# Performance work log

Measured on AMD Instinct MI355X. Metric: run time of the kernel, lower is better.

Reference implementation:

```python
import jax, jax.numpy as jnp
import numpy as np

DIM = 512
HID = 4 * DIM
E = 8
B, T = 2, 2048


def setup_inputs() -> dict:
    key = jax.random.key(0)
    ks = jax.random.split(key, 8)
    s = 0.02
    x = jax.random.normal(ks[0], (B, T, DIM), dtype=jnp.float32)
    route = jax.random.randint(ks[1], (B * T,), 0, E, dtype=jnp.int32)
    # stacked per-expert params; Linear y = x @ W + b with W in [in, out] layout
    w_in = jax.random.normal(ks[2], (E, DIM, HID), dtype=jnp.float32) * s
    b_in = jnp.zeros((E, HID), dtype=jnp.float32)
    w_gate = jax.random.normal(ks[3], (E, DIM, HID), dtype=jnp.float32) * s
    b_gate = jnp.zeros((E, HID), dtype=jnp.float32)
    w_out = jax.random.normal(ks[4], (E, HID, DIM), dtype=jnp.float32) * s
    b_out = jnp.zeros((E, DIM), dtype=jnp.float32)
    return {"x": x, "route": route, "w_in": w_in, "b_in": b_in,
            "w_gate": w_gate, "b_gate": b_gate, "w_out": w_out, "b_out": b_out}


def reference(x, route, w_in, b_in, w_gate, b_gate, w_out, b_out):
    Bb, Tt, C = x.shape
    xf = x.reshape(-1, C)  # [N, C]
    out = jnp.zeros_like(xf)
    n_experts = w_in.shape[0]
    # loop over the small fixed expert set; each expert is a SwiGLU FFN,
    # output scattered back by masking (same math as output[idx] += expert(x[idx]))
    for e in range(n_experts):
        mask = (route == e).astype(xf.dtype)[:, None]  # [N, 1]
        h = jax.nn.silu(xf @ w_gate[e] + b_gate[e]) * (xf @ w_in[e] + b_in[e])  # [N, 4C]
        out = out + mask * (h @ w_out[e] + b_out[e])
    return out.reshape(Bb, Tt, C)
```

## Files before the change

### kernel.cpp

```cpp
#include <hip/hip_runtime.h>

#define DIM 512
#define HID 2048
#define NEXP 8

typedef __attribute__((ext_vector_type(8))) short v8s;
typedef __attribute__((ext_vector_type(4))) float v4f;

__device__ __forceinline__ unsigned short f2bf(float f) {
  union { __bf16 b; unsigned short u; } c;
  c.b = (__bf16)f;
  return c.u;
}

__device__ __forceinline__ void gload16(const void* g, void* l) {
  __builtin_amdgcn_global_load_lds(
      (const __attribute__((address_space(1))) unsigned int*)g,
      (__attribute__((address_space(3))) unsigned int*)l, 16, 0, 0);
}

__global__ void route_prep(const int* __restrict__ route, int* __restrict__ meta, int ntok) {
  __shared__ int c[NEXP];
  int t = threadIdx.x;
  if (t < NEXP) c[t] = 0;
  __syncthreads();
  for (int n = t; n < ntok; n += blockDim.x) atomicAdd(&c[route[n]], 1);
  __syncthreads();
  if (t == 0) {
    int acc = 0, pacc = 0;
    for (int e = 0; e < NEXP; ++e) {
      meta[e] = c[e];
      meta[NEXP + e] = acc;
      meta[2 * NEXP + e] = acc;
      meta[3 * NEXP + e] = pacc;
      acc += c[e];
      pacc += ((c[e] + 127) >> 7) << 7;
    }
  }
}

__global__ void fill_perm(const int* __restrict__ route, int* __restrict__ meta,
                          int* __restrict__ perm, int ntok) {
  int n = blockIdx.x * blockDim.x + threadIdx.x;
  if (n < ntok) {
    int p = atomicAdd(&meta[2 * NEXP + route[n]], 1);
    perm[p] = n;
  }
}


__global__ __launch_bounds__(256) void wgi_conv(
    const float* __restrict__ wg, const float* __restrict__ wi,
    unsigned short* __restrict__ wgp, unsigned short* __restrict__ wip)
{
  const int s = blockIdx.x;
  const int j = blockIdx.y;
  const int e = blockIdx.z >> 1;
  const int which = blockIdx.z & 1;
  const float* src = (which ? wi : wg) + (size_t)e * DIM * HID;
  unsigned short* dst = (which ? wip : wgp) + (((size_t)e * 16 + j) * 8 + s) * 8192;
  const int t = threadIdx.x;
  #pragma unroll
  for (int i = 0; i < 4; ++i) {
    const int c = t + 256 * i;
    const int kq = c >> 7, n = c & 127;
    const float* srow = src + (size_t)(s * 64 + kq * 8) * HID + j * 128 + n;
    v8s r;
    #pragma unroll
    for (int q = 0; q < 8; ++q) r[q] = (short)f2bf(srow[(size_t)q * HID]);
    *(v8s*)(dst + (size_t)c * 8) = r;
  }
}

__global__ __launch_bounds__(256) void wo_conv(
    const float* __restrict__ wo, unsigned short* __restrict__ wop)
{
  const int s = blockIdx.x;
  const int j = blockIdx.y;
  const int e = blockIdx.z;
  const float* src = wo + (size_t)e * HID * DIM;
  unsigned short* dst = wop + (((size_t)e * 8 + j) * 32 + s) * 4096;
  const int t = threadIdx.x;
  #pragma unroll
  for (int i = 0; i < 2; ++i) {
    const int c = t + 256 * i;
    const int kq = c >> 6, n = c & 63;
    const float* srow = src + (size_t)(s * 64 + kq * 8) * DIM + j * 64 + n;
    v8s r;
    #pragma unroll
    for (int q = 0; q < 8; ++q) r[q] = (short)f2bf(srow[(size_t)q * DIM]);
    *(v8s*)(dst + (size_t)c * 8) = r;
  }
}

__global__ __launch_bounds__(256) void x_conv(
    const float* __restrict__ x, const int* __restrict__ meta,
    const int* __restrict__ perm, unsigned short* __restrict__ xp)
{
  const int bid = blockIdx.x;
  const int e = bid & 7;
  const int mt = bid >> 3;
  const int cnt = meta[e];
  if (mt * 64 >= cnt) return;
  const int off  = meta[NEXP + e];
  const int poff = meta[3 * NEXP + e];
  const int t = threadIdx.x;
  const int r = t & 63, q = t >> 6;
  int arow = mt * 64 + r; if (arow >= cnt) arow = cnt - 1;
  const float* src = x + (size_t)perm[off + arow] * DIM + q * 128;
  unsigned short* dst = xp + (size_t)((poff + mt * 64) >> 6) * 32768;
  #pragma unroll
  for (int j = 0; j < 16; ++j) {
    float4 f0 = ((const float4*)src)[2 * j];
    float4 f1 = ((const float4*)src)[2 * j + 1];
    v8s v;
    v[0] = (short)f2bf(f0.x); v[1] = (short)f2bf(f0.y);
    v[2] = (short)f2bf(f0.z); v[3] = (short)f2bf(f0.w);
    v[4] = (short)f2bf(f1.x); v[5] = (short)f2bf(f1.y);
    v[6] = (short)f2bf(f1.z); v[7] = (short)f2bf(f1.w);
    *(v8s*)(dst + (size_t)((q * 16 + j) * 64 + r) * 8) = v;
  }
}

__global__ __launch_bounds__(256, 4) void gemm1(
    const unsigned short* __restrict__ xp,
    const unsigned short* __restrict__ wgp, const float* __restrict__ bg_,
    const unsigned short* __restrict__ wip, const float* __restrict__ bi_,
    const int* __restrict__ meta,
    unsigned short* __restrict__ hbuf)
{
  const int bid = blockIdx.x;
  const int e = bid & 7;
  const int r_ = bid >> 3;
  const int j = r_ & 15;
  const int mt = r_ >> 4;
  const int cnt = meta[e];
  const int m0 = mt * 64;
  if (m0 >= cnt) return;
  const int poff = meta[3 * NEXP + e];
  const int n0 = j * 128;

  __shared__ __align__(16) unsigned char lds[40960];

  const int t = threadIdx.x;
  const int l = t & 63, w = t >> 6;
  const int wm = w >> 1, wn = w & 1;
  const int fr = l & 15, fg = l >> 4;

  const unsigned short* pa = xp + (size_t)((poff + m0) >> 6) * 32768;
  const unsigned short* pg = wgp + ((size_t)e * 16 + j) * 65536;
  const unsigned short* pi = wip + ((size_t)e * 16 + j) * 65536;

  v4f accG[2][4], accI[2][4];
  #pragma unroll
  for (int i = 0; i < 2; ++i)
    #pragma unroll
    for (int q = 0; q < 4; ++q) {
      accG[i][q] = (v4f){0.f, 0.f, 0.f, 0.f};
      accI[i][q] = (v4f){0.f, 0.f, 0.f, 0.f};
    }

  auto stage = [&](int s, int b) {
    unsigned char* base = lds + b * 20480;
    gload16(pa + (size_t)s * 2048 + t * 8,        base + w * 1024);
    gload16(pg + (size_t)s * 4096 + t * 8,        base + 4096 + w * 1024);
    gload16(pg + (size_t)s * 4096 + 2048 + t * 8, base + 8192 + w * 1024);
    gload16(pi + (size_t)s * 4096 + t * 8,        base + 12288 + w * 1024);
    gload16(pi + (size_t)s * 4096 + 2048 + t * 8, base + 16384 + w * 1024);
  };

  stage(0, 0);
  __syncthreads();

  int cur = 0;
  for (int s = 0; s < 16; ++s) {
    if (s < 15) stage(s + 1, cur ^ 1);
    unsigned char* base = lds + cur * 20480;
    v8s af[2], gf[4], inf[4];
    #pragma unroll
    for (int mf = 0; mf < 2; ++mf)
      af[mf] = *(const v8s*)(base + ((fg * 64) + wm * 32 + mf * 16 + fr) * 16);
    #pragma unroll
    for (int nf = 0; nf < 4; ++nf) {
      gf[nf]  = *(const v8s*)(base + 4096  + ((fg * 128) + wn * 64 + nf * 16 + fr) * 16);
      inf[nf] = *(const v8s*)(base + 12288 + ((fg * 128) + wn * 64 + nf * 16 + fr) * 16);
    }
    #pragma unroll
    for (int mf = 0; mf < 2; ++mf)
      #pragma unroll
      for (int nf = 0; nf < 4; ++nf) {
        accG[mf][nf] = __builtin_amdgcn_mfma_f32_16x16x32_bf16(af[mf], gf[nf],  accG[mf][nf], 0, 0, 0);
        accI[mf][nf] = __builtin_amdgcn_mfma_f32_16x16x32_bf16(af[mf], inf[nf], accI[mf][nf], 0, 0, 0);
      }
    __syncthreads();
    cur ^= 1;
  }

  const size_t tbase = (size_t)((poff + m0) >> 6) * 131072;
  #pragma unroll
  for (int nf = 0; nf < 4; ++nf) {
    const int c = n0 + wn * 64 + nf * 16 + fr;
    const float bg = bg_[(size_t)e * HID + c];
    const float bi = bi_[(size_t)e * HID + c];
    #pragma unroll
    for (int mf = 0; mf < 2; ++mf)
      #pragma unroll
      for (int jj = 0; jj < 4; ++jj) {
        const int r = wm * 32 + mf * 16 + fg * 4 + jj;
        if (m0 + r < cnt) {
          const float g = accG[mf][nf][jj] + bg;
          const float v = accI[mf][nf][jj] + bi;
          const float hval = g / (1.f + __expf(-g)) * v;
          hbuf[tbase + (size_t)((c >> 3) * 64 + r) * 8 + (c & 7)] = f2bf(hval);
        }
      }
  }
}

__global__ __launch_bounds__(512, 4) void gemm2(
    const unsigned short* __restrict__ hbuf,
    const unsigned short* __restrict__ wop, const float* __restrict__ bo_,
    const int* __restrict__ meta, const int* __restrict__ perm,
    float* __restrict__ out)
{
  const int bid = blockIdx.x;
  const int e = bid & 7;
  const int r_ = bid >> 3;
  const int jn = r_ & 7;
  const int mt = r_ >> 3;
  const int cnt = meta[e];
  const int m0 = mt * 64;
  if (m0 >= cnt) return;
  const int off  = meta[NEXP + e];
  const int poff = meta[3 * NEXP + e];
  const int n0 = jn * 64;

  __shared__ __align__(16) unsigned char lds[32768];

  const int t = threadIdx.x;
  const int l = t & 63, w = t >> 6;
  const int wm = w >> 2, wn = w & 3;
  const int fr = l & 15, fg = l >> 4;

  const unsigned short* pa = hbuf + (size_t)((poff + m0) >> 6) * 131072;
  const unsigned short* pb = wop + ((size_t)e * 8 + jn) * 131072;

  v4f acc[2];
  acc[0] = (v4f){0.f, 0.f, 0.f, 0.f};
  acc[1] = (v4f){0.f, 0.f, 0.f, 0.f};

  auto stage = [&](int s, int b) {
    unsigned char* base = lds + b * 16384;
    gload16(pa + (size_t)s * 4096 + t * 8, base + w * 1024);
    gload16(pb + (size_t)s * 4096 + t * 8, base + 8192 + w * 1024);
  };

  stage(0, 0);
  __syncthreads();

  int cur = 0;
  for (int s = 0; s < 32; ++s) {
    if (s < 31) stage(s + 1, cur ^ 1);
    unsigned char* base = lds + cur * 16384;
    v8s af[2][2], bf2[2];
    #pragma unroll
    for (int kk = 0; kk < 2; ++kk) {
      #pragma unroll
      for (int mf = 0; mf < 2; ++mf)
        af[kk][mf] = *(const v8s*)(base + ((kk * 4 + fg) * 64 + wm * 32 + mf * 16 + fr) * 16);
      bf2[kk] = *(const v8s*)(base + 8192 + ((kk * 4 + fg) * 64 + wn * 16 + fr) * 16);
    }
    #pragma unroll
    for (int kk = 0; kk < 2; ++kk)
      #pragma unroll
      for (int mf = 0; mf < 2; ++mf)
        acc[mf] = __builtin_amdgcn_mfma_f32_16x16x32_bf16(af[kk][mf], bf2[kk], acc[mf], 0, 0, 0);
    __syncthreads();
    cur ^= 1;
  }

  const int c = n0 + wn * 16 + fr;
  const float bo = bo_[(size_t)e * DIM + c];
  #pragma unroll
  for (int mf = 0; mf < 2; ++mf)
    #pragma unroll
    for (int jj = 0; jj < 4; ++jj) {
      const int r = wm * 32 + mf * 16 + fg * 4 + jj;
      if (m0 + r < cnt)
        out[(size_t)perm[off + m0 + r] * DIM + c] = acc[mf][jj] + bo;
    }
}

extern "C" void kernel_launch(void* const* d_in, const int* in_sizes, int n_in,
                              void* d_out, int out_size, void* d_ws, size_t ws_size,
                              hipStream_t stream) {
  const float* x      = (const float*)d_in[0];
  const int*   route  = (const int*)d_in[1];
  const float* w_in   = (const float*)d_in[2];
  const float* b_in   = (const float*)d_in[3];
  const float* w_gate = (const float*)d_in[4];
  const float* b_gate = (const float*)d_in[5];
  const float* w_out  = (const float*)d_in[6];
  const float* b_out  = (const float*)d_in[7];
  float* out = (float*)d_out;

  const int ntok = in_sizes[1];

  int* meta = (int*)d_ws;
  int* perm = (int*)((char*)d_ws + 128);

  const size_t WGP_OFF = 32768;
  const size_t WMAT_BYTES = (size_t)NEXP * DIM * HID * 2;

  unsigned short* wgp  = (unsigned short*)((char*)d_ws + WGP_OFF);
  unsigned short* wip  = (unsigned short*)((char*)d_ws + WGP_OFF + WMAT_BYTES);
  unsigned short* wop  = (unsigned short*)((char*)d_ws + WGP_OFF + 2 * WMAT_BYTES);
  unsigned short* xp   = wop;
  unsigned short* hbuf = (unsigned short*)((char*)d_ws + WGP_OFF + 3 * WMAT_BYTES);

  const int MT64 = (ntok + 63) / 64;

  route_prep<<<1, 256, 0, stream>>>(route, meta, ntok);
  fill_perm<<<(ntok + 255) / 256, 256, 0, stream>>>(route, meta, perm, ntok);
  x_conv<<<NEXP * MT64, 256, 0, stream>>>(x, meta, perm, xp);
  wgi_conv<<<dim3(8, 16, 16), 256, 0, stream>>>(w_gate, w_in, wgp, wip);
  gemm1<<<NEXP * 16 * MT64, 256, 0, stream>>>(
      xp, wgp, b_gate, wip, b_in, meta, hbuf);
  wo_conv<<<dim3(32, 8, 8), 256, 0, stream>>>(w_out, wop);
  gemm2<<<NEXP * 8 * MT64, 512, 0, stream>>>(
      hbuf, wop, b_out, meta, perm, out);
}
```

Measured before the change: 112.9 us.

## Fuse gate/in weight conversion into persistent LDS-resident gemm1 and enlarge gemm2 tiles

```diff
diff --git a/kernel.cpp b/kernel.cpp
--- a/kernel.cpp
+++ b/kernel.cpp
@@ -45,51 +45,6 @@
   if (n < ntok) {
     int p = atomicAdd(&meta[2 * NEXP + route[n]], 1);
     perm[p] = n;
-  }
-}
-
-
-__global__ __launch_bounds__(256) void wgi_conv(
-    const float* __restrict__ wg, const float* __restrict__ wi,
-    unsigned short* __restrict__ wgp, unsigned short* __restrict__ wip)
-{
-  const int s = blockIdx.x;
-  const int j = blockIdx.y;
-  const int e = blockIdx.z >> 1;
-  const int which = blockIdx.z & 1;
-  const float* src = (which ? wi : wg) + (size_t)e * DIM * HID;
-  unsigned short* dst = (which ? wip : wgp) + (((size_t)e * 16 + j) * 8 + s) * 8192;
-  const int t = threadIdx.x;
-  #pragma unroll
-  for (int i = 0; i < 4; ++i) {
-    const int c = t + 256 * i;
-    const int kq = c >> 7, n = c & 127;
-    const float* srow = src + (size_t)(s * 64 + kq * 8) * HID + j * 128 + n;
-    v8s r;
-    #pragma unroll
-    for (int q = 0; q < 8; ++q) r[q] = (short)f2bf(srow[(size_t)q * HID]);
-    *(v8s*)(dst + (size_t)c * 8) = r;
-  }
-}
-
-__global__ __launch_bounds__(256) void wo_conv(
-    const float* __restrict__ wo, unsigned short* __restrict__ wop)
-{
-  const int s = blockIdx.x;
-  const int j = blockIdx.y;
-  const int e = blockIdx.z;
-  const float* src = wo + (size_t)e * HID * DIM;
-  unsigned short* dst = wop + (((size_t)e * 8 + j) * 32 + s) * 4096;
-  const int t = threadIdx.x;
-  #pragma unroll
-  for (int i = 0; i < 2; ++i) {
-    const int c = t + 256 * i;
-    const int kq = c >> 6, n = c & 63;
-    const float* srow = src + (size_t)(s * 64 + kq * 8) * DIM + j * 64 + n;
-    v8s r;
-    #pragma unroll
-    for (int q = 0; q < 8; ++q) r[q] = (short)f2bf(srow[(size_t)q * DIM]);
-    *(v8s*)(dst + (size_t)c * 8) = r;
   }
 }
 
@@ -122,102 +77,141 @@
   }
 }
 
-__global__ __launch_bounds__(256, 4) void gemm1(
+__global__ __launch_bounds__(256) void wo_conv(
+    const float* __restrict__ wo, unsigned short* __restrict__ wop)
+{
+  const int s = blockIdx.x;
+  const int j = blockIdx.y;
+  const int e = blockIdx.z;
+  const float* src = wo + (size_t)e * HID * DIM;
+  unsigned short* dst = wop + (((size_t)e * 8 + j) * 32 + s) * 4096;
+  const int t = threadIdx.x;
+  #pragma unroll
+  for (int i = 0; i < 2; ++i) {
+    const int c = t + 256 * i;
+    const int kq = c >> 6, n = c & 63;
+    const float* srow = src + (size_t)(s * 64 + kq * 8) * DIM + j * 64 + n;
+    v8s r;
+    #pragma unroll
+    for (int q = 0; q < 8; ++q) r[q] = (short)f2bf(srow[(size_t)q * DIM]);
+    *(v8s*)(dst + (size_t)c * 8) = r;
+  }
+}
+
+__global__ __launch_bounds__(256, 1) void gemm1f(
     const unsigned short* __restrict__ xp,
-    const unsigned short* __restrict__ wgp, const float* __restrict__ bg_,
-    const unsigned short* __restrict__ wip, const float* __restrict__ bi_,
+    const float* __restrict__ wg_, const float* __restrict__ bg_,
+    const float* __restrict__ wi_, const float* __restrict__ bi_,
     const int* __restrict__ meta,
     unsigned short* __restrict__ hbuf)
 {
   const int bid = blockIdx.x;
   const int e = bid & 7;
-  const int r_ = bid >> 3;
-  const int j = r_ & 15;
-  const int mt = r_ >> 4;
+  const int j = bid >> 3;
+  const int n0 = j * 64;
   const int cnt = meta[e];
-  const int m0 = mt * 64;
-  if (m0 >= cnt) return;
   const int poff = meta[3 * NEXP + e];
-  const int n0 = j * 128;
-
-  __shared__ __align__(16) unsigned char lds[40960];
+
+  __shared__ __align__(16) unsigned char lds[163840];
 
   const int t = threadIdx.x;
   const int l = t & 63, w = t >> 6;
-  const int wm = w >> 1, wn = w & 1;
   const int fr = l & 15, fg = l >> 4;
 
-  const unsigned short* pa = xp + (size_t)((poff + m0) >> 6) * 32768;
-  const unsigned short* pg = wgp + ((size_t)e * 16 + j) * 65536;
-  const unsigned short* pi = wip + ((size_t)e * 16 + j) * 65536;
-
-  v4f accG[2][4], accI[2][4];
-  #pragma unroll
-  for (int i = 0; i < 2; ++i)
-    #pragma unroll
-    for (int q = 0; q < 4; ++q) {
-      accG[i][q] = (v4f){0.f, 0.f, 0.f, 0.f};
-      accI[i][q] = (v4f){0.f, 0.f, 0.f, 0.f};
-    }
-
-  auto stage = [&](int s, int b) {
-    unsigned char* base = lds + b * 20480;
-    gload16(pa + (size_t)s * 2048 + t * 8,        base + w * 1024);
-    gload16(pg + (size_t)s * 4096 + t * 8,        base + 4096 + w * 1024);
-    gload16(pg + (size_t)s * 4096 + 2048 + t * 8, base + 8192 + w * 1024);
-    gload16(pi + (size_t)s * 4096 + t * 8,        base + 12288 + w * 1024);
-    gload16(pi + (size_t)s * 4096 + 2048 + t * 8, base + 16384 + w * 1024);
-  };
-
-  stage(0, 0);
+  {
+    const float* wg = wg_ + (size_t)e * DIM * HID + n0 + l;
+    const float* wi = wi_ + (size_t)e * DIM * HID + n0 + l;
+    #pragma unroll 4
+    for (int it = 0; it < 16; ++it) {
+      const int kq = w + 4 * it;
+      const float* s0 = wg + (size_t)(kq * 8) * HID;
+      const float* s1 = wi + (size_t)(kq * 8) * HID;
+      v8s r0, r1;
+      #pragma unroll
+      for (int q = 0; q < 8; ++q) {
+        r0[q] = (short)f2bf(s0[(size_t)q * HID]);
+        r1[q] = (short)f2bf(s1[(size_t)q * HID]);
+      }
+      *(v8s*)(lds + (kq * 64 + l) * 16) = r0;
+      *(v8s*)(lds + 65536 + (kq * 64 + l) * 16) = r1;
+    }
+  }
   __syncthreads();
 
-  int cur = 0;
-  for (int s = 0; s < 16; ++s) {
-    if (s < 15) stage(s + 1, cur ^ 1);
-    unsigned char* base = lds + cur * 20480;
-    v8s af[2], gf[4], inf[4];
-    #pragma unroll
-    for (int mf = 0; mf < 2; ++mf)
-      af[mf] = *(const v8s*)(base + ((fg * 64) + wm * 32 + mf * 16 + fr) * 16);
+  unsigned char* xlds = lds + 131072;
+  const int tile0 = poff >> 6;
+  const int nmt = (cnt + 255) >> 8;
+
+  for (int mt = 0; mt < nmt; ++mt) {
+    const int m0 = mt * 256;
+    const size_t xbase = (size_t)(tile0 + (m0 >> 6)) * 32768;
+
+    auto stage_x = [&](int s, int b) {
+      #pragma unroll
+      for (int i = 0; i < 4; ++i)
+        gload16(xp + xbase + (size_t)w * 32768 + ((s * 4 + i) * 64 + l) * 8,
+                xlds + b * 16384 + (w * 64 + 256 * i) * 16);
+    };
+
+    stage_x(0, 0);
+    __syncthreads();
+
+    v4f aG[4][4], aI[4][4];
+    #pragma unroll
+    for (int i = 0; i < 4; ++i)
+      #pragma unroll
+      for (int q = 0; q < 4; ++q) {
+        aG[i][q] = (v4f){0.f, 0.f, 0.f, 0.f};
+        aI[i][q] = (v4f){0.f, 0.f, 0.f, 0.f};
+      }
+
+    int cur = 0;
+    for (int s = 0; s < 16; ++s) {
+      if (s < 15) stage_x(s + 1, cur ^ 1);
+      const unsigned char* xb = xlds + cur * 16384;
+      v8s af[4], gf[4], inf[4];
+      #pragma unroll
+      for (int mf = 0; mf < 4; ++mf)
+        af[mf] = *(const v8s*)(xb + (fg * 256 + w * 64 + mf * 16 + fr) * 16);
+      #pragma unroll
+      for (int nf = 0; nf < 4; ++nf) {
+        gf[nf]  = *(const v8s*)(lds + ((s * 4 + fg) * 64 + nf * 16 + fr) * 16);
+        inf[nf] = *(const v8s*)(lds + 65536 + ((s * 4 + fg) * 64 + nf * 16 + fr) * 16);
+      }
+      #pragma unroll
+      for (int mf = 0; mf < 4; ++mf)
+        #pragma unroll
+        for (int nf = 0; nf < 4; ++nf) {
+          aG[mf][nf] = __builtin_amdgcn_mfma_f32_16x16x32_bf16(af[mf], gf[nf],  aG[mf][nf], 0, 0, 0);
+          aI[mf][nf] = __builtin_amdgcn_mfma_f32_16x16x32_bf16(af[mf], inf[nf], aI[mf][nf], 0, 0, 0);
+        }
+      __syncthreads();
+      cur ^= 1;
+    }
+
     #pragma unroll
     for (int nf = 0; nf < 4; ++nf) {
-      gf[nf]  = *(const v8s*)(base + 4096  + ((fg * 128) + wn * 64 + nf * 16 + fr) * 16);
-      inf[nf] = *(const v8s*)(base + 12288 + ((fg * 128) + wn * 64 + nf * 16 + fr) * 16);
-    }
-    #pragma unroll
-    for (int mf = 0; mf < 2; ++mf)
-      #pragma unroll
-      for (int nf = 0; nf < 4; ++nf) {
-        accG[mf][nf] = __builtin_amdgcn_mfma_f32_16x16x32_bf16(af[mf], gf[nf],  accG[mf][nf], 0, 0, 0);
-        accI[mf][nf] = __builtin_amdgcn_mfma_f32_16x16x32_bf16(af[mf], inf[nf], accI[mf][nf], 0, 0, 0);
-      }
-    __syncthreads();
-    cur ^= 1;
-  }
-
-  const size_t tbase = (size_t)((poff + m0) >> 6) * 131072;
-  #pragma unroll
-  for (int nf = 0; nf < 4; ++nf) {
-    const int c = n0 + wn * 64 + nf * 16 + fr;
-    const float bg = bg_[(size_t)e * HID + c];
-    const float bi = bi_[(size_t)e * HID + c];
-    #pragma unroll
-    for (int mf = 0; mf < 2; ++mf)
-      #pragma unroll
-      for (int jj = 0; jj < 4; ++jj) {
-        const int r = wm * 32 + mf * 16 + fg * 4 + jj;
-        if (m0 + r < cnt) {
-          const float g = accG[mf][nf][jj] + bg;
-          const float v = accI[mf][nf][jj] + bi;
-          const float hval = g / (1.f + __expf(-g)) * v;
-          hbuf[tbase + (size_t)((c >> 3) * 64 + r) * 8 + (c & 7)] = f2bf(hval);
+      const int c = n0 + nf * 16 + fr;
+      const float bg = bg_[(size_t)e * HID + c];
+      const float bi = bi_[(size_t)e * HID + c];
+      #pragma unroll
+      for (int mf = 0; mf < 4; ++mf)
+        #pragma unroll
+        for (int jj = 0; jj < 4; ++jj) {
+          const int r = w * 64 + mf * 16 + fg * 4 + jj;
+          if (m0 + r < cnt) {
+            const float g = aG[mf][nf][jj] + bg;
+            const float v = aI[mf][nf][jj] + bi;
+            const float hval = g / (1.f + __expf(-g)) * v;
+            const int grow = poff + m0 + r;
+            hbuf[(size_t)(grow >> 6) * 131072 + ((c >> 3) * 64 + (grow & 63)) * 8 + (c & 7)] = f2bf(hval);
+          }
         }
-      }
-  }
-}
-
-__global__ __launch_bounds__(512, 4) void gemm2(
+    }
+  }
+}
+
+__global__ __launch_bounds__(256, 3) void gemm2n(
     const unsigned short* __restrict__ hbuf,
     const unsigned short* __restrict__ wop, const float* __restrict__ bo_,
     const int* __restrict__ meta, const int* __restrict__ perm,
@@ -229,30 +223,40 @@
   const int jn = r_ & 7;
   const int mt = r_ >> 3;
   const int cnt = meta[e];
-  const int m0 = mt * 64;
+  const int m0 = mt * 128;
   if (m0 >= cnt) return;
-  const int off  = meta[NEXP + e];
-  const int poff = meta[3 * NEXP + e];
+  const int off = meta[NEXP + e], poff = meta[3 * NEXP + e];
   const int n0 = jn * 64;
 
-  __shared__ __align__(16) unsigned char lds[32768];
+  __shared__ __align__(16) unsigned char lds[49152];
 
   const int t = threadIdx.x;
   const int l = t & 63, w = t >> 6;
-  const int wm = w >> 2, wn = w & 3;
+  const int wm = w >> 1, wn = w & 1;
   const int fr = l & 15, fg = l >> 4;
 
-  const unsigned short* pa = hbuf + (size_t)((poff + m0) >> 6) * 131072;
+  const size_t abase = (size_t)((poff + m0) >> 6) * 131072;
   const unsigned short* pb = wop + ((size_t)e * 8 + jn) * 131072;
 
-  v4f acc[2];
-  acc[0] = (v4f){0.f, 0.f, 0.f, 0.f};
-  acc[1] = (v4f){0.f, 0.f, 0.f, 0.f};
+  v4f acc[4][2];
+  #pragma unroll
+  for (int i = 0; i < 4; ++i) {
+    acc[i][0] = (v4f){0.f, 0.f, 0.f, 0.f};
+    acc[i][1] = (v4f){0.f, 0.f, 0.f, 0.f};
+  }
 
   auto stage = [&](int s, int b) {
-    unsigned char* base = lds + b * 16384;
-    gload16(pa + (size_t)s * 4096 + t * 8, base + w * 1024);
-    gload16(pb + (size_t)s * 4096 + t * 8, base + 8192 + w * 1024);
+    unsigned char* base = lds + b * 24576;
+    #pragma unroll
+    for (int i = 0; i < 4; ++i) {
+      const int kq = (4 * i + w) >> 1;
+      gload16(hbuf + abase + (size_t)(w & 1) * 131072 + ((s * 8 + kq) * 64 + l) * 8,
+              base + (w * 64 + 256 * i) * 16);
+    }
+    #pragma unroll
+    for (int i = 0; i < 2; ++i)
+      gload16(pb + (size_t)s * 4096 + (t + 256 * i) * 8,
+              base + 16384 + (w * 64 + 256 * i) * 16);
   };
 
   stage(0, 0);
@@ -261,34 +265,41 @@
   int cur = 0;
   for (int s = 0; s < 32; ++s) {
     if (s < 31) stage(s + 1, cur ^ 1);
-    unsigned char* base = lds + cur * 16384;
-    v8s af[2][2], bf2[2];
+    unsigned char* base = lds + cur * 24576;
+    v8s af[2][4], bf[2][2];
     #pragma unroll
     for (int kk = 0; kk < 2; ++kk) {
       #pragma unroll
-      for (int mf = 0; mf < 2; ++mf)
-        af[kk][mf] = *(const v8s*)(base + ((kk * 4 + fg) * 64 + wm * 32 + mf * 16 + fr) * 16);
-      bf2[kk] = *(const v8s*)(base + 8192 + ((kk * 4 + fg) * 64 + wn * 16 + fr) * 16);
+      for (int mf = 0; mf < 4; ++mf)
+        af[kk][mf] = *(const v8s*)(base + ((kk * 4 + fg) * 128 + wm * 64 + mf * 16 + fr) * 16);
+      #pragma unroll
+      for (int nf = 0; nf < 2; ++nf)
+        bf[kk][nf] = *(const v8s*)(base + 16384 + ((kk * 4 + fg) * 64 + wn * 32 + nf * 16 + fr) * 16);
     }
     #pragma unroll
     for (int kk = 0; kk < 2; ++kk)
       #pragma unroll
-      for (int mf = 0; mf < 2; ++mf)
-        acc[mf] = __builtin_amdgcn_mfma_f32_16x16x32_bf16(af[kk][mf], bf2[kk], acc[mf], 0, 0, 0);
+      for (int mf = 0; mf < 4; ++mf)
+        #pragma unroll
+        for (int nf = 0; nf < 2; ++nf)
+          acc[mf][nf] = __builtin_amdgcn_mfma_f32_16x16x32_bf16(af[kk][mf], bf[kk][nf], acc[mf][nf], 0, 0, 0);
     __syncthreads();
     cur ^= 1;
   }
 
-  const int c = n0 + wn * 16 + fr;
-  const float bo = bo_[(size_t)e * DIM + c];
   #pragma unroll
-  for (int mf = 0; mf < 2; ++mf)
-    #pragma unroll
-    for (int jj = 0; jj < 4; ++jj) {
-      const int r = wm * 32 + mf * 16 + fg * 4 + jj;
-      if (m0 + r < cnt)
-        out[(size_t)perm[off + m0 + r] * DIM + c] = acc[mf][jj] + bo;
-    }
+  for (int nf = 0; nf < 2; ++nf) {
+    const int c = n0 + wn * 32 + nf * 16 + fr;
+    const float bo = bo_[(size_t)e * DIM + c];
+    #pragma unroll
+    for (int mf = 0; mf < 4; ++mf)
+      #pragma unroll
+      for (int jj = 0; jj < 4; ++jj) {
+        const int r = wm * 64 + mf * 16 + fg * 4 + jj;
+        if (m0 + r < cnt)
+          out[(size_t)perm[off + m0 + r] * DIM + c] = acc[mf][nf][jj] + bo;
+      }
+  }
 }
 
 extern "C" void kernel_launch(void* const* d_in, const int* in_sizes, int n_in,
@@ -309,24 +320,19 @@
   int* meta = (int*)d_ws;
   int* perm = (int*)((char*)d_ws + 128);
 
-  const size_t WGP_OFF = 32768;
-  const size_t WMAT_BYTES = (size_t)NEXP * DIM * HID * 2;
-
-  unsigned short* wgp  = (unsigned short*)((char*)d_ws + WGP_OFF);
-  unsigned short* wip  = (unsigned short*)((char*)d_ws + WGP_OFF + WMAT_BYTES);
-  unsigned short* wop  = (unsigned short*)((char*)d_ws + WGP_OFF + 2 * WMAT_BYTES);
-  unsigned short* xp   = wop;
-  unsigned short* hbuf = (unsigned short*)((char*)d_ws + WGP_OFF + 3 * WMAT_BYTES);
-
-  const int MT64 = (ntok + 63) / 64;
+  unsigned short* xp   = (unsigned short*)((char*)d_ws + 65536);
+  unsigned short* wop  = (unsigned short*)((char*)d_ws + 65536 + 5242880);
+  unsigned short* hbuf = (unsigned short*)((char*)d_ws + 65536 + 5242880 + 33554432);
+
+  const int MT64  = (ntok + 63) / 64;
+  const int MT128 = (ntok + 127) / 128;
 
   route_prep<<<1, 256, 0, stream>>>(route, meta, ntok);
   fill_perm<<<(ntok + 255) / 256, 256, 0, stream>>>(route, meta, perm, ntok);
   x_conv<<<NEXP * MT64, 256, 0, stream>>>(x, meta, perm, xp);
-  wgi_conv<<<dim3(8, 16, 16), 256, 0, stream>>>(w_gate, w_in, wgp, wip);
-  gemm1<<<NEXP * 16 * MT64, 256, 0, stream>>>(
-      xp, wgp, b_gate, wip, b_in, meta, hbuf);
+  gemm1f<<<NEXP * 32, 256, 0, stream>>>(
+      xp, w_gate, b_gate, w_in, b_in, meta, hbuf);
   wo_conv<<<dim3(32, 8, 8), 256, 0, stream>>>(w_out, wop);
-  gemm2<<<NEXP * 8 * MT64, 512, 0, stream>>>(
+  gemm2n<<<NEXP * 8 * MT128, 256, 0, stream>>>(
       hbuf, wop, b_out, meta, perm, out);
 }
```

New measurement: 124.9 us. 10.6% more time.

## Fuse fp32-to-bf16 weight conversion into the expert GEMM load stages

Applied to the files above, without the earlier changes.

```diff
diff --git a/kernel.cpp b/kernel.cpp
--- a/kernel.cpp
+++ b/kernel.cpp
@@ -45,51 +45,6 @@
   if (n < ntok) {
     int p = atomicAdd(&meta[2 * NEXP + route[n]], 1);
     perm[p] = n;
-  }
-}
-
-
-__global__ __launch_bounds__(256) void wgi_conv(
-    const float* __restrict__ wg, const float* __restrict__ wi,
-    unsigned short* __restrict__ wgp, unsigned short* __restrict__ wip)
-{
-  const int s = blockIdx.x;
-  const int j = blockIdx.y;
-  const int e = blockIdx.z >> 1;
-  const int which = blockIdx.z & 1;
-  const float* src = (which ? wi : wg) + (size_t)e * DIM * HID;
-  unsigned short* dst = (which ? wip : wgp) + (((size_t)e * 16 + j) * 8 + s) * 8192;
-  const int t = threadIdx.x;
-  #pragma unroll
-  for (int i = 0; i < 4; ++i) {
-    const int c = t + 256 * i;
-    const int kq = c >> 7, n = c & 127;
-    const float* srow = src + (size_t)(s * 64 + kq * 8) * HID + j * 128 + n;
-    v8s r;
-    #pragma unroll
-    for (int q = 0; q < 8; ++q) r[q] = (short)f2bf(srow[(size_t)q * HID]);
-    *(v8s*)(dst + (size_t)c * 8) = r;
-  }
-}
-
-__global__ __launch_bounds__(256) void wo_conv(
-    const float* __restrict__ wo, unsigned short* __restrict__ wop)
-{
-  const int s = blockIdx.x;
-  const int j = blockIdx.y;
-  const int e = blockIdx.z;
-  const float* src = wo + (size_t)e * HID * DIM;
-  unsigned short* dst = wop + (((size_t)e * 8 + j) * 32 + s) * 4096;
-  const int t = threadIdx.x;
-  #pragma unroll
-  for (int i = 0; i < 2; ++i) {
-    const int c = t + 256 * i;
-    const int kq = c >> 6, n = c & 63;
-    const float* srow = src + (size_t)(s * 64 + kq * 8) * DIM + j * 64 + n;
-    v8s r;
-    #pragma unroll
-    for (int q = 0; q < 8; ++q) r[q] = (short)f2bf(srow[(size_t)q * DIM]);
-    *(v8s*)(dst + (size_t)c * 8) = r;
   }
 }
 
@@ -122,10 +77,10 @@
   }
 }
 
-__global__ __launch_bounds__(256, 4) void gemm1(
+__global__ __launch_bounds__(256, 3) void gemm1r(
     const unsigned short* __restrict__ xp,
-    const unsigned short* __restrict__ wgp, const float* __restrict__ bg_,
-    const unsigned short* __restrict__ wip, const float* __restrict__ bi_,
+    const float* __restrict__ wg_, const float* __restrict__ bg_,
+    const float* __restrict__ wi_, const float* __restrict__ bi_,
     const int* __restrict__ meta,
     unsigned short* __restrict__ hbuf)
 {
@@ -148,55 +103,82 @@
   const int fr = l & 15, fg = l >> 4;
 
   const unsigned short* pa = xp + (size_t)((poff + m0) >> 6) * 32768;
-  const unsigned short* pg = wgp + ((size_t)e * 16 + j) * 65536;
-  const unsigned short* pi = wip + ((size_t)e * 16 + j) * 65536;
-
-  v4f accG[2][4], accI[2][4];
+  const float* wg = wg_ + (size_t)e * DIM * HID + n0;
+  const float* wi = wi_ + (size_t)e * DIM * HID + n0;
+
+  const int s_kq = t >> 7;
+  const int s_n  = t & 127;
+
+  v4f aG[2][4], aI[2][4];
   #pragma unroll
   for (int i = 0; i < 2; ++i)
     #pragma unroll
     for (int q = 0; q < 4; ++q) {
-      accG[i][q] = (v4f){0.f, 0.f, 0.f, 0.f};
-      accI[i][q] = (v4f){0.f, 0.f, 0.f, 0.f};
-    }
-
-  auto stage = [&](int s, int b) {
+      aG[i][q] = (v4f){0.f, 0.f, 0.f, 0.f};
+      aI[i][q] = (v4f){0.f, 0.f, 0.f, 0.f};
+    }
+
+  float stG0[8], stG1[8], stI0[8], stI1[8];
+
+  auto wload = [&](int s) {
+    const size_t b0 = (size_t)(s * 32 + s_kq * 8) * HID + s_n;
+    const size_t b1 = (size_t)(s * 32 + (s_kq + 2) * 8) * HID + s_n;
+    #pragma unroll
+    for (int q = 0; q < 8; ++q) {
+      stG0[q] = wg[b0 + (size_t)q * HID];
+      stG1[q] = wg[b1 + (size_t)q * HID];
+      stI0[q] = wi[b0 + (size_t)q * HID];
+      stI1[q] = wi[b1 + (size_t)q * HID];
+    }
+  };
+  auto wstore = [&](int b) {
     unsigned char* base = lds + b * 20480;
-    gload16(pa + (size_t)s * 2048 + t * 8,        base + w * 1024);
-    gload16(pg + (size_t)s * 4096 + t * 8,        base + 4096 + w * 1024);
-    gload16(pg + (size_t)s * 4096 + 2048 + t * 8, base + 8192 + w * 1024);
-    gload16(pi + (size_t)s * 4096 + t * 8,        base + 12288 + w * 1024);
-    gload16(pi + (size_t)s * 4096 + 2048 + t * 8, base + 16384 + w * 1024);
-  };
-
-  stage(0, 0);
+    v8s g0, g1, i0, i1;
+    #pragma unroll
+    for (int q = 0; q < 8; ++q) {
+      g0[q] = (short)f2bf(stG0[q]); g1[q] = (short)f2bf(stG1[q]);
+      i0[q] = (short)f2bf(stI0[q]); i1[q] = (short)f2bf(stI1[q]);
+    }
+    *(v8s*)(base + 4096  + (s_kq * 128 + s_n) * 16)       = g0;
+    *(v8s*)(base + 4096  + ((s_kq + 2) * 128 + s_n) * 16) = g1;
+    *(v8s*)(base + 12288 + (s_kq * 128 + s_n) * 16)       = i0;
+    *(v8s*)(base + 12288 + ((s_kq + 2) * 128 + s_n) * 16) = i1;
+  };
+  auto aload = [&](int s, int b) {
+    gload16(pa + ((size_t)(s * 4 + w) * 64 + l) * 8, lds + b * 20480 + t * 16);
+  };
+
+  wload(0);
+  aload(0, 0);
+  wstore(0);
   __syncthreads();
 
   int cur = 0;
   for (int s = 0; s < 16; ++s) {
-    if (s < 15) stage(s + 1, cur ^ 1);
-    unsigned char* base = lds + cur * 20480;
+    if (s < 15) { wload(s + 1); aload(s + 1, cur ^ 1); }
+    const unsigned char* base = lds + cur * 20480;
     v8s af[2], gf[4], inf[4];
     #pragma unroll
     for (int mf = 0; mf < 2; ++mf)
-      af[mf] = *(const v8s*)(base + ((fg * 64) + wm * 32 + mf * 16 + fr) * 16);
+      af[mf] = *(const v8s*)(base + (fg * 64 + wm * 32 + mf * 16 + fr) * 16);
     #pragma unroll
     for (int nf = 0; nf < 4; ++nf) {
-      gf[nf]  = *(const v8s*)(base + 4096  + ((fg * 128) + wn * 64 + nf * 16 + fr) * 16);
-      inf[nf] = *(const v8s*)(base + 12288 + ((fg * 128) + wn * 64 + nf * 16 + fr) * 16);
+      gf[nf]  = *(const v8s*)(base + 4096  + (fg * 128 + wn * 64 + nf * 16 + fr) * 16);
+      inf[nf] = *(const v8s*)(base + 12288 + (fg * 128 + wn * 64 + nf * 16 + fr) * 16);
     }
     #pragma unroll
     for (int mf = 0; mf < 2; ++mf)
       #pragma unroll
       for (int nf = 0; nf < 4; ++nf) {
-        accG[mf][nf] = __builtin_amdgcn_mfma_f32_16x16x32_bf16(af[mf], gf[nf],  accG[mf][nf], 0, 0, 0);
-        accI[mf][nf] = __builtin_amdgcn_mfma_f32_16x16x32_bf16(af[mf], inf[nf], accI[mf][nf], 0, 0, 0);
+        aG[mf][nf] = __builtin_amdgcn_mfma_f32_16x16x32_bf16(af[mf], gf[nf],  aG[mf][nf], 0, 0, 0);
+        aI[mf][nf] = __builtin_amdgcn_mfma_f32_16x16x32_bf16(af[mf], inf[nf], aI[mf][nf], 0, 0, 0);
       }
+    if (s < 15) wstore(cur ^ 1);
     __syncthreads();
     cur ^= 1;
   }
 
-  const size_t tbase = (size_t)((poff + m0) >> 6) * 131072;
+  const size_t tb = (size_t)((poff + m0) >> 6) * 131072;
   #pragma unroll
   for (int nf = 0; nf < 4; ++nf) {
     const int c = n0 + wn * 64 + nf * 16 + fr;
@@ -207,74 +189,89 @@
       #pragma unroll
       for (int jj = 0; jj < 4; ++jj) {
         const int r = wm * 32 + mf * 16 + fg * 4 + jj;
-        if (m0 + r < cnt) {
-          const float g = accG[mf][nf][jj] + bg;
-          const float v = accI[mf][nf][jj] + bi;
-          const float hval = g / (1.f + __expf(-g)) * v;
-          hbuf[tbase + (size_t)((c >> 3) * 64 + r) * 8 + (c & 7)] = f2bf(hval);
-        }
+        const float g = aG[mf][nf][jj] + bg;
+        const float v = aI[mf][nf][jj] + bi;
+        const float hval = g / (1.f + __expf(-g)) * v;
+        hbuf[tb + (size_t)((c >> 3) * 64 + r) * 8 + (c & 7)] = f2bf(hval);
       }
   }
 }
 
-__global__ __launch_bounds__(512, 4) void gemm2(
+__global__ __launch_bounds__(256, 4) void gemm2r(
     const unsigned short* __restrict__ hbuf,
-    const unsigned short* __restrict__ wop, const float* __restrict__ bo_,
+    const float* __restrict__ wo_, const float* __restrict__ bo_,
     const int* __restrict__ meta, const int* __restrict__ perm,
     float* __restrict__ out)
 {
   const int bid = blockIdx.x;
   const int e = bid & 7;
   const int r_ = bid >> 3;
-  const int jn = r_ & 7;
-  const int mt = r_ >> 3;
+  const int jn = r_ & 15;
+  const int mt = r_ >> 4;
   const int cnt = meta[e];
   const int m0 = mt * 64;
   if (m0 >= cnt) return;
-  const int off  = meta[NEXP + e];
-  const int poff = meta[3 * NEXP + e];
-  const int n0 = jn * 64;
-
-  __shared__ __align__(16) unsigned char lds[32768];
+  const int off = meta[NEXP + e], poff = meta[3 * NEXP + e];
+  const int n0 = jn * 32;
+
+  __shared__ __align__(16) unsigned char lds[24576];
 
   const int t = threadIdx.x;
   const int l = t & 63, w = t >> 6;
-  const int wm = w >> 2, wn = w & 3;
+  const int wm = w >> 1, wn = w & 1;
   const int fr = l & 15, fg = l >> 4;
 
   const unsigned short* pa = hbuf + (size_t)((poff + m0) >> 6) * 131072;
-  const unsigned short* pb = wop + ((size_t)e * 8 + jn) * 131072;
+  const float* wo = wo_ + (size_t)e * HID * DIM + n0;
+
+  const int b_kq = t >> 5, b_n = t & 31;
 
   v4f acc[2];
   acc[0] = (v4f){0.f, 0.f, 0.f, 0.f};
   acc[1] = (v4f){0.f, 0.f, 0.f, 0.f};
 
-  auto stage = [&](int s, int b) {
-    unsigned char* base = lds + b * 16384;
-    gload16(pa + (size_t)s * 4096 + t * 8, base + w * 1024);
-    gload16(pb + (size_t)s * 4096 + t * 8, base + 8192 + w * 1024);
-  };
-
-  stage(0, 0);
+  float stB[8];
+  auto bload = [&](int s) {
+    const size_t b0 = (size_t)(s * 64 + b_kq * 8) * DIM + b_n;
+    #pragma unroll
+    for (int q = 0; q < 8; ++q) stB[q] = wo[b0 + (size_t)q * DIM];
+  };
+  auto bstore = [&](int b) {
+    v8s r;
+    #pragma unroll
+    for (int q = 0; q < 8; ++q) r[q] = (short)f2bf(stB[q]);
+    *(v8s*)(lds + b * 12288 + 8192 + (b_kq * 32 + b_n) * 16) = r;
+  };
+  auto aload = [&](int s, int b) {
+    #pragma unroll
+    for (int i = 0; i < 2; ++i)
+      gload16(pa + (size_t)s * 4096 + ((size_t)(i * 4 + w) * 64 + l) * 8,
+              lds + b * 12288 + ((i * 4 + w) * 64) * 16 + l * 16);
+  };
+
+  bload(0);
+  aload(0, 0);
+  bstore(0);
   __syncthreads();
 
   int cur = 0;
   for (int s = 0; s < 32; ++s) {
-    if (s < 31) stage(s + 1, cur ^ 1);
-    unsigned char* base = lds + cur * 16384;
-    v8s af[2][2], bf2[2];
+    if (s < 31) { bload(s + 1); aload(s + 1, cur ^ 1); }
+    const unsigned char* base = lds + cur * 12288;
+    v8s af[2][2], bf[2];
     #pragma unroll
     for (int kk = 0; kk < 2; ++kk) {
       #pragma unroll
       for (int mf = 0; mf < 2; ++mf)
         af[kk][mf] = *(const v8s*)(base + ((kk * 4 + fg) * 64 + wm * 32 + mf * 16 + fr) * 16);
-      bf2[kk] = *(const v8s*)(base + 8192 + ((kk * 4 + fg) * 64 + wn * 16 + fr) * 16);
+      bf[kk] = *(const v8s*)(base + 8192 + ((kk * 4 + fg) * 32 + wn * 16 + fr) * 16);
     }
     #pragma unroll
     for (int kk = 0; kk < 2; ++kk)
       #pragma unroll
       for (int mf = 0; mf < 2; ++mf)
-        acc[mf] = __builtin_amdgcn_mfma_f32_16x16x32_bf16(af[kk][mf], bf2[kk], acc[mf], 0, 0, 0);
+        acc[mf] = __builtin_amdgcn_mfma_f32_16x16x32_bf16(af[kk][mf], bf[kk], acc[mf], 0, 0, 0);
+    if (s < 31) bstore(cur ^ 1);
     __syncthreads();
     cur ^= 1;
   }
@@ -309,24 +306,16 @@
   int* meta = (int*)d_ws;
   int* perm = (int*)((char*)d_ws + 128);
 
-  const size_t WGP_OFF = 32768;
-  const size_t WMAT_BYTES = (size_t)NEXP * DIM * HID * 2;
-
-  unsigned short* wgp  = (unsigned short*)((char*)d_ws + WGP_OFF);
-  unsigned short* wip  = (unsigned short*)((char*)d_ws + WGP_OFF + WMAT_BYTES);
-  unsigned short* wop  = (unsigned short*)((char*)d_ws + WGP_OFF + 2 * WMAT_BYTES);
-  unsigned short* xp   = wop;
-  unsigned short* hbuf = (unsigned short*)((char*)d_ws + WGP_OFF + 3 * WMAT_BYTES);
+  unsigned short* xp   = (unsigned short*)((char*)d_ws + 65536);
+  unsigned short* hbuf = (unsigned short*)((char*)d_ws + 65536 + 5242880);
 
   const int MT64 = (ntok + 63) / 64;
 
   route_prep<<<1, 256, 0, stream>>>(route, meta, ntok);
   fill_perm<<<(ntok + 255) / 256, 256, 0, stream>>>(route, meta, perm, ntok);
   x_conv<<<NEXP * MT64, 256, 0, stream>>>(x, meta, perm, xp);
-  wgi_conv<<<dim3(8, 16, 16), 256, 0, stream>>>(w_gate, w_in, wgp, wip);
-  gemm1<<<NEXP * 16 * MT64, 256, 0, stream>>>(
-      xp, wgp, b_gate, wip, b_in, meta, hbuf);
-  wo_conv<<<dim3(32, 8, 8), 256, 0, stream>>>(w_out, wop);
-  gemm2<<<NEXP * 8 * MT64, 512, 0, stream>>>(
-      hbuf, wop, b_out, meta, perm, out);
-}
+  gemm1r<<<NEXP * 16 * MT64, 256, 0, stream>>>(
+      xp, w_gate, b_gate, w_in, b_in, meta, hbuf);
+  gemm2r<<<NEXP * 16 * MT64, 256, 0, stream>>>(
+      hbuf, w_out, b_out, meta, perm, out);
+}
```

Result: faster. 110.5 us (-2.2%).

## Retile expert GEMMs with 128-row tiles and stripe-major block order

Applied to the files above, without the earlier changes.

```diff
diff --git a/kernel.cpp b/kernel.cpp
--- a/kernel.cpp
+++ b/kernel.cpp
@@ -48,51 +48,6 @@
   }
 }
 
-
-__global__ __launch_bounds__(256) void wgi_conv(
-    const float* __restrict__ wg, const float* __restrict__ wi,
-    unsigned short* __restrict__ wgp, unsigned short* __restrict__ wip)
-{
-  const int s = blockIdx.x;
-  const int j = blockIdx.y;
-  const int e = blockIdx.z >> 1;
-  const int which = blockIdx.z & 1;
-  const float* src = (which ? wi : wg) + (size_t)e * DIM * HID;
-  unsigned short* dst = (which ? wip : wgp) + (((size_t)e * 16 + j) * 8 + s) * 8192;
-  const int t = threadIdx.x;
-  #pragma unroll
-  for (int i = 0; i < 4; ++i) {
-    const int c = t + 256 * i;
-    const int kq = c >> 7, n = c & 127;
-    const float* srow = src + (size_t)(s * 64 + kq * 8) * HID + j * 128 + n;
-    v8s r;
-    #pragma unroll
-    for (int q = 0; q < 8; ++q) r[q] = (short)f2bf(srow[(size_t)q * HID]);
-    *(v8s*)(dst + (size_t)c * 8) = r;
-  }
-}
-
-__global__ __launch_bounds__(256) void wo_conv(
-    const float* __restrict__ wo, unsigned short* __restrict__ wop)
-{
-  const int s = blockIdx.x;
-  const int j = blockIdx.y;
-  const int e = blockIdx.z;
-  const float* src = wo + (size_t)e * HID * DIM;
-  unsigned short* dst = wop + (((size_t)e * 8 + j) * 32 + s) * 4096;
-  const int t = threadIdx.x;
-  #pragma unroll
-  for (int i = 0; i < 2; ++i) {
-    const int c = t + 256 * i;
-    const int kq = c >> 6, n = c & 63;
-    const float* srow = src + (size_t)(s * 64 + kq * 8) * DIM + j * 64 + n;
-    v8s r;
-    #pragma unroll
-    for (int q = 0; q < 8; ++q) r[q] = (short)f2bf(srow[(size_t)q * DIM]);
-    *(v8s*)(dst + (size_t)c * 8) = r;
-  }
-}
-
 __global__ __launch_bounds__(256) void x_conv(
     const float* __restrict__ x, const int* __restrict__ meta,
     const int* __restrict__ perm, unsigned short* __restrict__ xp)
@@ -101,7 +56,8 @@
   const int e = bid & 7;
   const int mt = bid >> 3;
   const int cnt = meta[e];
-  if (mt * 64 >= cnt) return;
+  const int padded = ((cnt + 127) >> 7) << 7;
+  if (mt * 64 >= padded) return;
   const int off  = meta[NEXP + e];
   const int poff = meta[3 * NEXP + e];
   const int t = threadIdx.x;
@@ -122,7 +78,51 @@
   }
 }
 
-__global__ __launch_bounds__(256, 4) void gemm1(
+__global__ __launch_bounds__(256) void wgi_conv(
+    const float* __restrict__ wg, const float* __restrict__ wi,
+    unsigned short* __restrict__ wgp, unsigned short* __restrict__ wip)
+{
+  const int s = blockIdx.x;
+  const int j = blockIdx.y;
+  const int e = blockIdx.z >> 1;
+  const int which = blockIdx.z & 1;
+  const float* src = (which ? wi : wg) + (size_t)e * DIM * HID;
+  unsigned short* dst = (which ? wip : wgp) + (((size_t)e * 16 + j) * 8 + s) * 8192;
+  const int t = threadIdx.x;
+  #pragma unroll
+  for (int i = 0; i < 4; ++i) {
+    const int c = t + 256 * i;
+    const int kq = c >> 7, n = c & 127;
+    const float* srow = src + (size_t)(s * 64 + kq * 8) * HID + j * 128 + n;
+    v8s r;
+    #pragma unroll
+    for (int q = 0; q < 8; ++q) r[q] = (short)f2bf(srow[(size_t)q * HID]);
+    *(v8s*)(dst + (size_t)c * 8) = r;
+  }
+}
+
+__global__ __launch_bounds__(256) void wo_conv(
+    const float* __restrict__ wo, unsigned short* __restrict__ wop)
+{
+  const int s = blockIdx.x;
+  const int j = blockIdx.y;
+  const int e = blockIdx.z;
+  const float* src = wo + (size_t)e * HID * DIM;
+  unsigned short* dst = wop + (((size_t)e * 8 + j) * 32 + s) * 4096;
+  const int t = threadIdx.x;
+  #pragma unroll
+  for (int i = 0; i < 2; ++i) {
+    const int c = t + 256 * i;
+    const int kq = c >> 6, n = c & 63;
+    const float* srow = src + (size_t)(s * 64 + kq * 8) * DIM + j * 64 + n;
+    v8s r;
+    #pragma unroll
+    for (int q = 0; q < 8; ++q) r[q] = (short)f2bf(srow[(size_t)q * DIM]);
+    *(v8s*)(dst + (size_t)c * 8) = r;
+  }
+}
+
+__global__ __launch_bounds__(256, 4) void gemm1g(
     const unsigned short* __restrict__ xp,
     const unsigned short* __restrict__ wgp, const float* __restrict__ bg_,
     const unsigned short* __restrict__ wip, const float* __restrict__ bi_,
@@ -130,43 +130,49 @@
     unsigned short* __restrict__ hbuf)
 {
   const int bid = blockIdx.x;
-  const int e = bid & 7;
-  const int r_ = bid >> 3;
-  const int j = r_ & 15;
-  const int mt = r_ >> 4;
+  const int stripe = bid & 255;
+  const int mt = bid >> 8;
+  const int e = stripe >> 5, j = stripe & 31;
   const int cnt = meta[e];
-  const int m0 = mt * 64;
+  const int m0 = mt * 128;
   if (m0 >= cnt) return;
   const int poff = meta[3 * NEXP + e];
-  const int n0 = j * 128;
-
-  __shared__ __align__(16) unsigned char lds[40960];
+  const int n0 = j * 64;
+
+  __shared__ __align__(16) unsigned char lds[32768];
 
   const int t = threadIdx.x;
   const int l = t & 63, w = t >> 6;
   const int wm = w >> 1, wn = w & 1;
   const int fr = l & 15, fg = l >> 4;
 
-  const unsigned short* pa = xp + (size_t)((poff + m0) >> 6) * 32768;
-  const unsigned short* pg = wgp + ((size_t)e * 16 + j) * 65536;
-  const unsigned short* pi = wip + ((size_t)e * 16 + j) * 65536;
-
-  v4f accG[2][4], accI[2][4];
-  #pragma unroll
-  for (int i = 0; i < 2; ++i)
-    #pragma unroll
-    for (int q = 0; q < 4; ++q) {
-      accG[i][q] = (v4f){0.f, 0.f, 0.f, 0.f};
-      accI[i][q] = (v4f){0.f, 0.f, 0.f, 0.f};
+  const int tile0 = (poff + m0) >> 6;
+  const int half = j & 1;
+  const unsigned short* pg = wgp + ((size_t)e * 16 + (j >> 1)) * 65536;
+  const unsigned short* pi = wip + ((size_t)e * 16 + (j >> 1)) * 65536;
+
+  const int aq0 = t >> 7, am0 = t & 127;
+  const int aq1 = (t + 256) >> 7, am1 = t & 127;
+  const int gq = t >> 6, gn = t & 63;
+
+  v4f aG[4][2], aI[4][2];
+  #pragma unroll
+  for (int i = 0; i < 4; ++i)
+    #pragma unroll
+    for (int q = 0; q < 2; ++q) {
+      aG[i][q] = (v4f){0.f, 0.f, 0.f, 0.f};
+      aI[i][q] = (v4f){0.f, 0.f, 0.f, 0.f};
     }
 
   auto stage = [&](int s, int b) {
-    unsigned char* base = lds + b * 20480;
-    gload16(pa + (size_t)s * 2048 + t * 8,        base + w * 1024);
-    gload16(pg + (size_t)s * 4096 + t * 8,        base + 4096 + w * 1024);
-    gload16(pg + (size_t)s * 4096 + 2048 + t * 8, base + 8192 + w * 1024);
-    gload16(pi + (size_t)s * 4096 + t * 8,        base + 12288 + w * 1024);
-    gload16(pi + (size_t)s * 4096 + 2048 + t * 8, base + 16384 + w * 1024);
+    unsigned char* base = lds + b * 16384;
+    gload16(xp + (size_t)(tile0 + (am0 >> 6)) * 32768 + ((size_t)(s * 4 + aq0) * 64 + (am0 & 63)) * 8,
+            base + t * 16);
+    gload16(xp + (size_t)(tile0 + (am1 >> 6)) * 32768 + ((size_t)(s * 4 + aq1) * 64 + (am1 & 63)) * 8,
+            base + (t + 256) * 16);
+    const size_t woff = (size_t)(s >> 1) * 8192 + ((size_t)((s & 1) * 4 + gq) * 128 + half * 64 + gn) * 8;
+    gload16(pg + woff, base + 8192 + t * 16);
+    gload16(pi + woff, base + 12288 + t * 16);
   };
 
   stage(0, 0);
@@ -175,84 +181,91 @@
   int cur = 0;
   for (int s = 0; s < 16; ++s) {
     if (s < 15) stage(s + 1, cur ^ 1);
-    unsigned char* base = lds + cur * 20480;
-    v8s af[2], gf[4], inf[4];
-    #pragma unroll
-    for (int mf = 0; mf < 2; ++mf)
-      af[mf] = *(const v8s*)(base + ((fg * 64) + wm * 32 + mf * 16 + fr) * 16);
-    #pragma unroll
-    for (int nf = 0; nf < 4; ++nf) {
-      gf[nf]  = *(const v8s*)(base + 4096  + ((fg * 128) + wn * 64 + nf * 16 + fr) * 16);
-      inf[nf] = *(const v8s*)(base + 12288 + ((fg * 128) + wn * 64 + nf * 16 + fr) * 16);
-    }
-    #pragma unroll
-    for (int mf = 0; mf < 2; ++mf)
-      #pragma unroll
-      for (int nf = 0; nf < 4; ++nf) {
-        accG[mf][nf] = __builtin_amdgcn_mfma_f32_16x16x32_bf16(af[mf], gf[nf],  accG[mf][nf], 0, 0, 0);
-        accI[mf][nf] = __builtin_amdgcn_mfma_f32_16x16x32_bf16(af[mf], inf[nf], accI[mf][nf], 0, 0, 0);
+    const unsigned char* base = lds + cur * 16384;
+    v8s af[4], gf[2], inf[2];
+    #pragma unroll
+    for (int mf = 0; mf < 4; ++mf)
+      af[mf] = *(const v8s*)(base + (fg * 128 + wm * 64 + mf * 16 + fr) * 16);
+    #pragma unroll
+    for (int nf = 0; nf < 2; ++nf) {
+      gf[nf]  = *(const v8s*)(base + 8192  + (fg * 64 + wn * 32 + nf * 16 + fr) * 16);
+      inf[nf] = *(const v8s*)(base + 12288 + (fg * 64 + wn * 32 + nf * 16 + fr) * 16);
+    }
+    #pragma unroll
+    for (int mf = 0; mf < 4; ++mf)
+      #pragma unroll
+      for (int nf = 0; nf < 2; ++nf) {
+        aG[mf][nf] = __builtin_amdgcn_mfma_f32_16x16x32_bf16(af[mf], gf[nf],  aG[mf][nf], 0, 0, 0);
+        aI[mf][nf] = __builtin_amdgcn_mfma_f32_16x16x32_bf16(af[mf], inf[nf], aI[mf][nf], 0, 0, 0);
       }
     __syncthreads();
     cur ^= 1;
   }
 
-  const size_t tbase = (size_t)((poff + m0) >> 6) * 131072;
-  #pragma unroll
-  for (int nf = 0; nf < 4; ++nf) {
-    const int c = n0 + wn * 64 + nf * 16 + fr;
+  #pragma unroll
+  for (int nf = 0; nf < 2; ++nf) {
+    const int c = n0 + wn * 32 + nf * 16 + fr;
     const float bg = bg_[(size_t)e * HID + c];
     const float bi = bi_[(size_t)e * HID + c];
     #pragma unroll
-    for (int mf = 0; mf < 2; ++mf)
+    for (int mf = 0; mf < 4; ++mf)
       #pragma unroll
       for (int jj = 0; jj < 4; ++jj) {
-        const int r = wm * 32 + mf * 16 + fg * 4 + jj;
-        if (m0 + r < cnt) {
-          const float g = accG[mf][nf][jj] + bg;
-          const float v = accI[mf][nf][jj] + bi;
-          const float hval = g / (1.f + __expf(-g)) * v;
-          hbuf[tbase + (size_t)((c >> 3) * 64 + r) * 8 + (c & 7)] = f2bf(hval);
-        }
+        const int r = wm * 64 + mf * 16 + fg * 4 + jj;
+        const float g = aG[mf][nf][jj] + bg;
+        const float v = aI[mf][nf][jj] + bi;
+        const float hval = g / (1.f + __expf(-g)) * v;
+        const int grow = poff + m0 + r;
+        hbuf[(size_t)(grow >> 6) * 131072 + ((size_t)(c >> 3) * 64 + (grow & 63)) * 8 + (c & 7)] = f2bf(hval);
       }
   }
 }
 
-__global__ __launch_bounds__(512, 4) void gemm2(
+__global__ __launch_bounds__(256, 4) void gemm2g(
     const unsigned short* __restrict__ hbuf,
     const unsigned short* __restrict__ wop, const float* __restrict__ bo_,
     const int* __restrict__ meta, const int* __restrict__ perm,
     float* __restrict__ out)
 {
   const int bid = blockIdx.x;
-  const int e = bid & 7;
-  const int r_ = bid >> 3;
-  const int jn = r_ & 7;
-  const int mt = r_ >> 3;
+  const int stripe = bid & 63;
+  const int mt = bid >> 6;
+  const int e = stripe >> 3, jn = stripe & 7;
   const int cnt = meta[e];
   const int m0 = mt * 64;
   if (m0 >= cnt) return;
-  const int off  = meta[NEXP + e];
-  const int poff = meta[3 * NEXP + e];
+  const int off = meta[NEXP + e], poff = meta[3 * NEXP + e];
   const int n0 = jn * 64;
 
   __shared__ __align__(16) unsigned char lds[32768];
 
   const int t = threadIdx.x;
   const int l = t & 63, w = t >> 6;
-  const int wm = w >> 2, wn = w & 3;
+  const int wm = w >> 1, wn = w & 1;
   const int fr = l & 15, fg = l >> 4;
 
   const unsigned short* pa = hbuf + (size_t)((poff + m0) >> 6) * 131072;
   const unsigned short* pb = wop + ((size_t)e * 8 + jn) * 131072;
 
-  v4f acc[2];
-  acc[0] = (v4f){0.f, 0.f, 0.f, 0.f};
-  acc[1] = (v4f){0.f, 0.f, 0.f, 0.f};
+  v4f acc[2][2];
+  #pragma unroll
+  for (int i = 0; i < 2; ++i) {
+    acc[i][0] = (v4f){0.f, 0.f, 0.f, 0.f};
+    acc[i][1] = (v4f){0.f, 0.f, 0.f, 0.f};
+  }
 
   auto stage = [&](int s, int b) {
     unsigned char* base = lds + b * 16384;
-    gload16(pa + (size_t)s * 4096 + t * 8, base + w * 1024);
-    gload16(pb + (size_t)s * 4096 + t * 8, base + 8192 + w * 1024);
+    #pragma unroll
+    for (int i = 0; i < 2; ++i) {
+      const int c = t + 256 * i;
+      gload16(pa + (size_t)s * 4096 + (size_t)c * 8, base + c * 16);
+    }
+    #pragma unroll
+    for (int i = 0; i < 2; ++i) {
+      const int c = t + 256 * i;
+      gload16(pb + (size_t)s * 4096 + (size_t)c * 8, base + 8192 + c * 16);
+    }
   };
 
   stage(0, 0);
@@ -261,34 +274,39 @@
   int cur = 0;
   for (int s = 0; s < 32; ++s) {
     if (s < 31) stage(s + 1, cur ^ 1);
-    unsigned char* base = lds + cur * 16384;
-    v8s af[2][2], bf2[2];
+    const unsigned char* base = lds + cur * 16384;
     #pragma unroll
     for (int kk = 0; kk < 2; ++kk) {
+      v8s af[2], bf[2];
       #pragma unroll
       for (int mf = 0; mf < 2; ++mf)
-        af[kk][mf] = *(const v8s*)(base + ((kk * 4 + fg) * 64 + wm * 32 + mf * 16 + fr) * 16);
-      bf2[kk] = *(const v8s*)(base + 8192 + ((kk * 4 + fg) * 64 + wn * 16 + fr) * 16);
-    }
-    #pragma unroll
-    for (int kk = 0; kk < 2; ++kk)
+        af[mf] = *(const v8s*)(base + ((kk * 4 + fg) * 64 + wm * 32 + mf * 16 + fr) * 16);
+      #pragma unroll
+      for (int nf = 0; nf < 2; ++nf)
+        bf[nf] = *(const v8s*)(base + 8192 + ((kk * 4 + fg) * 64 + wn * 32 + nf * 16 + fr) * 16);
       #pragma unroll
       for (int mf = 0; mf < 2; ++mf)
-        acc[mf] = __builtin_amdgcn_mfma_f32_16x16x32_bf16(af[kk][mf], bf2[kk], acc[mf], 0, 0, 0);
+        #pragma unroll
+        for (int nf = 0; nf < 2; ++nf)
+          acc[mf][nf] = __builtin_amdgcn_mfma_f32_16x16x32_bf16(af[mf], bf[nf], acc[mf][nf], 0, 0, 0);
+    }
     __syncthreads();
     cur ^= 1;
   }
 
-  const int c = n0 + wn * 16 + fr;
-  const float bo = bo_[(size_t)e * DIM + c];
-  #pragma unroll
-  for (int mf = 0; mf < 2; ++mf)
-    #pragma unroll
-    for (int jj = 0; jj < 4; ++jj) {
-      const int r = wm * 32 + mf * 16 + fg * 4 + jj;
-      if (m0 + r < cnt)
-        out[(size_t)perm[off + m0 + r] * DIM + c] = acc[mf][jj] + bo;
-    }
+  #pragma unroll
+  for (int nf = 0; nf < 2; ++nf) {
+    const int c = n0 + wn * 32 + nf * 16 + fr;
+    const float bo = bo_[(size_t)e * DIM + c];
+    #pragma unroll
+    for (int mf = 0; mf < 2; ++mf)
+      #pragma unroll
+      for (int jj = 0; jj < 4; ++jj) {
+        const int r = wm * 32 + mf * 16 + fg * 4 + jj;
+        if (m0 + r < cnt)
+          out[(size_t)perm[off + m0 + r] * DIM + c] = acc[mf][nf][jj] + bo;
+      }
+  }
 }
 
 extern "C" void kernel_launch(void* const* d_in, const int* in_sizes, int n_in,
@@ -309,24 +327,24 @@
   int* meta = (int*)d_ws;
   int* perm = (int*)((char*)d_ws + 128);
 
-  const size_t WGP_OFF = 32768;
-  const size_t WMAT_BYTES = (size_t)NEXP * DIM * HID * 2;
-
-  unsigned short* wgp  = (unsigned short*)((char*)d_ws + WGP_OFF);
-  unsigned short* wip  = (unsigned short*)((char*)d_ws + WGP_OFF + WMAT_BYTES);
-  unsigned short* wop  = (unsigned short*)((char*)d_ws + WGP_OFF + 2 * WMAT_BYTES);
-  unsigned short* xp   = wop;
-  unsigned short* hbuf = (unsigned short*)((char*)d_ws + WGP_OFF + 3 * WMAT_BYTES);
-
-  const int MT64 = (ntok + 63) / 64;
+  const size_t W_OFF  = 65536;
+  const size_t WMAT   = (size_t)NEXP * DIM * HID * 2;
+  unsigned short* wgp  = (unsigned short*)((char*)d_ws + W_OFF);
+  unsigned short* wip  = (unsigned short*)((char*)d_ws + W_OFF + WMAT);
+  unsigned short* wop  = wgp;
+  unsigned short* xp   = (unsigned short*)((char*)d_ws + W_OFF + 2 * WMAT);
+  unsigned short* hbuf = (unsigned short*)((char*)d_ws + W_OFF + 2 * WMAT + 5242880);
+
+  const int MT64  = (ntok + 63) / 64;
+  const int MT128 = (ntok + 127) / 128;
 
   route_prep<<<1, 256, 0, stream>>>(route, meta, ntok);
   fill_perm<<<(ntok + 255) / 256, 256, 0, stream>>>(route, meta, perm, ntok);
   x_conv<<<NEXP * MT64, 256, 0, stream>>>(x, meta, perm, xp);
   wgi_conv<<<dim3(8, 16, 16), 256, 0, stream>>>(w_gate, w_in, wgp, wip);
-  gemm1<<<NEXP * 16 * MT64, 256, 0, stream>>>(
+  gemm1g<<<256 * MT128, 256, 0, stream>>>(
       xp, wgp, b_gate, wip, b_in, meta, hbuf);
   wo_conv<<<dim3(32, 8, 8), 256, 0, stream>>>(w_out, wop);
-  gemm2<<<NEXP * 8 * MT64, 512, 0, stream>>>(
+  gemm2g<<<64 * MT64, 256, 0, stream>>>(
       hbuf, wop, b_out, meta, perm, out);
 }
```

New measurement: 119.5 us. +5.8%, slower.
